# Kernel optimization log

Measured on AMD Instinct MI355X. Metric: run time of the kernel, lower is better.

## Reference

```python
import jax, jax.numpy as jnp
import numpy as np

N, M = 1024, 32
FN, FE = 64, 32
AGG_N, AGG_E = 128, 64
OUT_N, OUT_E = 64, 32


def _build_indices(n, m):
    nip, eip = [], []
    k = 0
    for i in range(1, n):
        j0 = max(0, i - m)
        nip += list(range(j0, i))
        eip += list(range(k, k + i - j0))
        k += i - j0
    n1 = np.array(nip, np.int32)
    eT = np.array(eip, np.int32)
    n2 = np.concatenate([np.full(min(i, m), i, np.int32) for i in range(1, n)])
    # padded previous-node window indices (0 = zero pad slot)
    prev_nodes = np.zeros(n * m, np.int32)
    k = 0
    for i in range(n):
        t = min(i, m)
        prev_nodes[(i + 1) * m - t:(i + 1) * m] = np.arange(k, k + t) + 1
        k += t
    n_e = k
    norm_node = np.full(n, 1.0 / m, np.float32)
    for i in range(1, m):
        norm_node[i] = 1.0 / i
    prev_edges = np.zeros(n_e * m, np.int32)
    k = 0
    e = 0
    for i in range(n):
        j0 = max(0, i - m)
        for j in range(j0, i):
            if j > j0:
                prev_edges[(e + 1) * m - (j - j0):(e + 1) * m] = np.arange(k, k + j - j0) + 1
            e += 1
        k += i - j0
    norm_edge = np.ones(n_e, np.float32)
    k = 0
    for i in range(1, n):
        t = min(i, m)
        for j in range(t):
            if j > 0:
                norm_edge[k] = 1.0 / j
            k += 1
    return n1, eT, n2, prev_nodes, norm_node, prev_edges, norm_edge, n_e

N1, ET, N2, PREV_N, NORM_N, PREV_E, NORM_E, NE = _build_indices(N, M)
N1 = jnp.asarray(N1); ET = jnp.asarray(ET); N2 = jnp.asarray(N2)
PREV_N = jnp.asarray(PREV_N); PREV_E = jnp.asarray(PREV_E)
NORM_N = jnp.asarray(NORM_N); NORM_E = jnp.asarray(NORM_E)


def setup_inputs() -> dict:
    key = jax.random.key(0)
    ks = jax.random.split(key, 20)
    s = 0.02
    inp = {
        'input_nodes': jax.random.normal(ks[0], (2, N, FN), jnp.float32),
        'input_edges': jax.random.normal(ks[1], (2, NE, FE), jnp.float32),
        # node-branch MLPs (exclude_last=False)
        'Wan1': jax.random.normal(ks[2], (2 * FN + FE, 2 * AGG_N)) * s,
        'ban1': jnp.zeros((2 * AGG_N,)),
        'Wan2': jax.random.normal(ks[3], (2 * AGG_N, AGG_N)) * s,
        'ban2': jnp.zeros((AGG_N,)),
        'Wln1': jax.random.normal(ks[4], (AGG_N + FN, AGG_N + FN)) * s,
        'bln1': jnp.zeros((AGG_N + FN,)),
        'Wln2': jax.random.normal(ks[5], (AGG_N + FN, OUT_N)) * s,
        'bln2': jnp.zeros((OUT_N,)),
        # edge-branch MLPs
        'Wae1': jax.random.normal(ks[6], (FN + FE, 2 * AGG_E)) * s,
        'bae1': jnp.zeros((2 * AGG_E,)),
        'Wae2': jax.random.normal(ks[7], (2 * AGG_E, AGG_E)) * s,
        'bae2': jnp.zeros((AGG_E,)),
        'Wle1': jax.random.normal(ks[8], (AGG_E + FE, AGG_E + FE)) * s,
        'ble1': jnp.zeros((AGG_E + FE,)),
        'Wle2': jax.random.normal(ks[9], (AGG_E + FE, OUT_E)) * s,
        'ble2': jnp.zeros((OUT_E,)),
    }
    return inp


def _mlp2(x, W1, b1, W2, b2):
    return jax.nn.relu(jax.nn.relu(x @ W1 + b1) @ W2 + b2)


def reference(input_nodes, input_edges, Wan1, ban1, Wan2, ban2, Wln1, bln1, Wln2, bln2,
              Wae1, bae1, Wae2, bae2, Wle1, ble1, Wle2, ble2):
    B = input_nodes.shape[0]
    # gather node-edge pairs [B, NE, FN+FE] and node-edge-node triples [B, NE, 2FN+FE]
    pairs = jnp.concatenate([input_nodes[:, N1], input_edges[:, ET]], axis=-1)
    triples = jnp.concatenate([input_nodes[:, N1], input_edges[:, ET], input_nodes[:, N2]], axis=-1)
    # node branch (exclude_last=False -> triples)
    hn = _mlp2(triples, Wan1, ban1, Wan2, ban2)                     # [B, NE, AGG_N]
    hn = jnp.concatenate([jnp.zeros((B, 1, AGG_N), hn.dtype), hn], axis=1)
    pn = hn[:, PREV_N].reshape(B, N, M, AGG_N).sum(axis=2)          # padded window sum
    pn = pn * NORM_N[None, :, None]
    nodes_in = jnp.concatenate([pn, input_nodes], axis=-1)
    out_nodes = _mlp2(nodes_in, Wln1, bln1, Wln2, bln2)             # activation_nodes = relu
    # edge branch (pairs)
    he = _mlp2(pairs, Wae1, bae1, Wae2, bae2)                       # [B, NE, AGG_E]
    he = jnp.concatenate([jnp.zeros((B, 1, AGG_E), he.dtype), he], axis=1)
    pe = he[:, PREV_E].reshape(B, NE, M, AGG_E).sum(axis=2)
    pe = pe * NORM_E[None, :, None]
    edges_in = jnp.concatenate([pe, input_edges], axis=-1)
    out_edges = _mlp2(edges_in, Wle1, ble1, Wle2, ble2)             # activation_edges = relu
    return out_nodes, out_edges
```

## Files before the change

kernel.cpp:

```cpp
#include <hip/hip_runtime.h>
#include <cstdint>

#define NN    1024
#define MM    32
#define NEDGE 32240
#define MROWS 64480
#define PX    168
#define PSTN  264
#define PXE   104
#define PH1   136
#define PHE   72

typedef unsigned short ushort_t;

typedef __bf16 bf16x8 __attribute__((ext_vector_type(8)));
typedef float  floatx4 __attribute__((ext_vector_type(4)));

__device__ __forceinline__ float b2f(ushort_t u) {
    union { unsigned int i; float f; } v; v.i = ((unsigned int)u) << 16; return v.f;
}
__device__ __forceinline__ ushort_t f2b(float f) {
    unsigned int u = __builtin_bit_cast(unsigned int, f);
    u = (u + 0x7FFFu + ((u >> 16) & 1u)) >> 16;
    return (ushort_t)u;
}
__device__ __forceinline__ int edge_base(int i) {
    return (i <= MM) ? ((i * (i - 1)) >> 1) : (496 + (i - MM) * MM);
}

__global__ __launch_bounds__(256) void k_pack(
        const float* an1, const float* an2, const float* ae1, const float* ae2,
        const float* le1, const float* le2, const float* ln1, const float* ln2,
        const float* nodes, const float* edges,
        ushort_t* pan1, ushort_t* pan2, ushort_t* pae1, ushort_t* pae2,
        ushort_t* ple1, ushort_t* ple2, ushort_t* pln1, ushort_t* pln2,
        ushort_t* nodesb, ushort_t* edgesb) {
    __shared__ float tile[32][33];
    const int bid = blockIdx.x;
    const int tid = threadIdx.x;
    if (bid < 152) {
        const float* s; ushort_t* d; int K, N, t;
        if (bid < 40)       { s = an1; d = pan1; K = 160; N = 256; t = bid;       }
        else if (bid < 72)  { s = an2; d = pan2; K = 256; N = 128; t = bid - 40;  }
        else if (bid < 84)  { s = ae1; d = pae1; K = 96;  N = 128; t = bid - 72;  }
        else if (bid < 92)  { s = ae2; d = pae2; K = 128; N = 64;  t = bid - 84;  }
        else if (bid < 101) { s = le1; d = ple1; K = 96;  N = 96;  t = bid - 92;  }
        else if (bid < 104) { s = le2; d = ple2; K = 96;  N = 32;  t = bid - 101; }
        else if (bid < 140) { s = ln1; d = pln1; K = 192; N = 192; t = bid - 104; }
        else                { s = ln2; d = pln2; K = 192; N = 64;  t = bid - 140; }
        int ntn = N >> 5;
        int tk = t / ntn, tn = t - tk * ntn;
        int k0 = tk * 32, n0 = tn * 32;
        int tx = tid & 31, ty = tid >> 5;
#pragma unroll
        for (int m = 0; m < 4; ++m)
            tile[ty + m * 8][tx] = s[(size_t)(k0 + ty + m * 8) * N + n0 + tx];
        __syncthreads();
#pragma unroll
        for (int m = 0; m < 4; ++m)
            d[(size_t)(n0 + ty + m * 8) * K + k0 + tx] = f2b(tile[tx][ty + m * 8]);
    } else if (bid < 280) {
        int i4 = (bid - 152) * 256 + tid;
        float4 v = ((const float4*)nodes)[i4];
        uint2 o;
        o.x = (unsigned)f2b(v.x) | ((unsigned)f2b(v.y) << 16);
        o.y = (unsigned)f2b(v.z) | ((unsigned)f2b(v.w) << 16);
        ((uint2*)nodesb)[i4] = o;
    } else {
        int i4 = (bid - 280) * 256 + tid;
        if (i4 < 515840) {
            float4 v = ((const float4*)edges)[i4];
            uint2 o;
            o.x = (unsigned)f2b(v.x) | ((unsigned)f2b(v.y) << 16);
            o.y = (unsigned)f2b(v.z) | ((unsigned)f2b(v.w) << 16);
            ((uint2*)edgesb)[i4] = o;
        }
    }
}

__global__ __launch_bounds__(512, 4) void k_main(
        const ushort_t* __restrict__ nodesb, const ushort_t* __restrict__ edgesb,
        const ushort_t* __restrict__ pan1, const float* __restrict__ ban1,
        const ushort_t* __restrict__ pan2, const float* __restrict__ ban2,
        const ushort_t* __restrict__ pae1, const float* __restrict__ bae1,
        const ushort_t* __restrict__ pae2, const float* __restrict__ bae2,
        const ushort_t* __restrict__ ple1, const float* __restrict__ ble1,
        const ushort_t* __restrict__ ple2, const float* __restrict__ ble2,
        ushort_t* __restrict__ pn, float* __restrict__ out_edges) {
    __shared__ alignas(16) ushort_t SH[26624];
    const int tid = threadIdx.x;
    const int w = tid >> 6, l = tid & 63, lrow = l & 15, lq = l >> 4;
    const int bid = blockIdx.x;
    floatx4 zero = {0.f, 0.f, 0.f, 0.f};

    if (bid < 2048) {
        const int b = bid >> 10, i = bid & 1023;
        const int t = min(i, MM);
        if (i == 0) {
            if (tid < 64) ((unsigned*)(pn + (size_t)bid * 128))[tid] = 0u;
            return;
        }
        const int j0 = i - t;
        const int base = b * NEDGE + edge_base(i);
        ushort_t* X = SH;
        ushort_t* H = SH + 32 * PX;

        bf16x8 B0[5], B1[5];
#pragma unroll
        for (int kt = 0; kt < 5; ++kt) {
            B0[kt] = *(const bf16x8*)(pan1 + (size_t)(16 * w + lrow) * 160 + kt * 32 + lq * 8);
            B1[kt] = *(const bf16x8*)(pan1 + (size_t)(16 * (w + 8) + lrow) * 160 + kt * 32 + lq * 8);
        }
        float c0 = ban1[16 * w + lrow];
        float c1 = ban1[16 * (w + 8) + lrow];

#pragma unroll
        for (int k = 0; k < 4; ++k) {
            int rr = w * 4 + k;
            unsigned* xr = (unsigned*)(X + rr * PX);
            const unsigned* nj = (const unsigned*)(nodesb + (size_t)(b * NN + j0 + rr) * 64);
            const unsigned* ni = (const unsigned*)(nodesb + (size_t)(b * NN + i) * 64);
            const unsigned* eb = (const unsigned*)(edgesb + (size_t)(base + rr) * 32);
            if (l < 32) { xr[l] = nj[l]; xr[48 + l] = ni[l]; }
            else        xr[l] = eb[l - 32];
        }
        __syncthreads();

#pragma unroll
        for (int s = 0; s < 2; ++s) {
            bf16x8 A[5];
#pragma unroll
            for (int kt = 0; kt < 5; ++kt)
                A[kt] = *(const bf16x8*)&X[(s * 16 + lrow) * PX + kt * 32 + lq * 8];
            floatx4 a0 = zero, a1 = zero;
#pragma unroll
            for (int kt = 0; kt < 5; ++kt) {
                a0 = __builtin_amdgcn_mfma_f32_16x16x32_bf16(A[kt], B0[kt], a0, 0, 0, 0);
                a1 = __builtin_amdgcn_mfma_f32_16x16x32_bf16(A[kt], B1[kt], a1, 0, 0, 0);
            }
#pragma unroll
            for (int r_ = 0; r_ < 4; ++r_) {
                int row = (s * 16 + lq * 4 + r_) * PSTN;
                H[row + 16 * w + lrow]       = f2b(fmaxf(a0[r_] + c0, 0.f));
                H[row + 128 + 16 * w + lrow] = f2b(fmaxf(a1[r_] + c1, 0.f));
            }
        }
        __syncthreads();

        {
            bf16x8 D[8];
#pragma unroll
            for (int kt = 0; kt < 8; ++kt)
                D[kt] = *(const bf16x8*)(pan2 + (size_t)(16 * w + lrow) * 256 + kt * 32 + lq * 8);
            float d0 = ban2[16 * w + lrow];
#pragma unroll
            for (int s = 0; s < 2; ++s) {
                floatx4 a0 = zero;
#pragma unroll
                for (int kt = 0; kt < 8; ++kt) {
                    bf16x8 a = *(const bf16x8*)&H[(s * 16 + lrow) * PSTN + kt * 32 + lq * 8];
                    a0 = __builtin_amdgcn_mfma_f32_16x16x32_bf16(a, D[kt], a0, 0, 0, 0);
                }
#pragma unroll
                for (int r_ = 0; r_ < 4; ++r_)
                    X[(s * 16 + lq * 4 + r_) * 136 + 16 * w + lrow] = f2b(fmaxf(a0[r_] + d0, 0.f));
            }
        }
        __syncthreads();

        {
            int c = tid & 63, g = tid >> 6;
            float s0 = 0.f, s1 = 0.f;
            for (int p = g; p < t; p += 8) {
                unsigned u = ((const unsigned*)X)[p * 68 + c];
                s0 += b2f((ushort_t)(u & 0xffff));
                s1 += b2f((ushort_t)(u >> 16));
            }
            float* red = (float*)(SH + 32 * PX);
            red[g * 128 + 2 * c]     = s0;
            red[g * 128 + 2 * c + 1] = s1;
            __syncthreads();
            if (tid < 64) {
                float inv = 1.0f / (float)t;
                float a0 = 0.f, a1 = 0.f;
#pragma unroll
                for (int g2 = 0; g2 < 8; ++g2) {
                    a0 += red[g2 * 128 + 2 * tid];
                    a1 += red[g2 * 128 + 2 * tid + 1];
                }
                a0 *= inv; a1 *= inv;
                ((unsigned*)(pn + (size_t)bid * 128))[tid] =
                    (unsigned)f2b(a0) | ((unsigned)f2b(a1) << 16);
            }
        }
    } else {
        const int q = bid - 2048;
        const int h = w >> 2, w4 = w & 3;
        const int lt = tid & 255;
        const int ri = 2 * q + h;
        const int b = ri >> 10, i = ri & 1023;
        const int t = min(i, MM);
        const int j0 = i - t;
        const int base = b * NEDGE + edge_base(i);
        ushort_t* Xe = SH + h * 13312;
        ushort_t* H1 = Xe + 3328;
        ushort_t* HE = H1 + 4352;
        ushort_t* LB = HE + 2304;

        bf16x8 B0[3], B1[3];
#pragma unroll
        for (int kt = 0; kt < 3; ++kt) {
            B0[kt] = *(const bf16x8*)(pae1 + (size_t)(16 * w4 + lrow) * 96 + kt * 32 + lq * 8);
            B1[kt] = *(const bf16x8*)(pae1 + (size_t)(16 * (w4 + 4) + lrow) * 96 + kt * 32 + lq * 8);
        }
        const float c0 = bae1[16 * w4 + lrow];
        const float c1 = bae1[16 * (w4 + 4) + lrow];

        for (int u = lt; u < 32 * 48; u += 256) {
            int row = u / 48, c = u - row * 48;
            unsigned v;
            if (c < 32) v = ((const unsigned*)nodesb)[(size_t)(b * NN + j0 + row) * 32 + c];
            else        v = ((const unsigned*)edgesb)[(size_t)(base + row) * 16 + (c - 32)];
            ((unsigned*)Xe)[row * (PXE / 2) + c] = v;
        }
        __syncthreads();

#pragma unroll
        for (int s = 0; s < 2; ++s) {
            bf16x8 A[3];
#pragma unroll
            for (int kt = 0; kt < 3; ++kt)
                A[kt] = *(const bf16x8*)&Xe[(s * 16 + lrow) * PXE + kt * 32 + lq * 8];
            floatx4 a0 = zero, a1 = zero;
#pragma unroll
            for (int kt = 0; kt < 3; ++kt) {
                a0 = __builtin_amdgcn_mfma_f32_16x16x32_bf16(A[kt], B0[kt], a0, 0, 0, 0);
                a1 = __builtin_amdgcn_mfma_f32_16x16x32_bf16(A[kt], B1[kt], a1, 0, 0, 0);
            }
#pragma unroll
            for (int r_ = 0; r_ < 4; ++r_) {
                int row = (s * 16 + lq * 4 + r_) * PH1;
                H1[row + 16 * w4 + lrow]      = f2b(fmaxf(a0[r_] + c0, 0.f));
                H1[row + 64 + 16 * w4 + lrow] = f2b(fmaxf(a1[r_] + c1, 0.f));
            }
        }
        __syncthreads();

        {
            bf16x8 E[4];
#pragma unroll
            for (int kt = 0; kt < 4; ++kt)
                E[kt] = *(const bf16x8*)(pae2 + (size_t)(16 * w4 + lrow) * 128 + kt * 32 + lq * 8);
            float d2 = bae2[16 * w4 + lrow];
#pragma unroll
            for (int s = 0; s < 2; ++s) {
                floatx4 a2 = zero;
#pragma unroll
                for (int kt = 0; kt < 4; ++kt) {
                    bf16x8 a = *(const bf16x8*)&H1[(s * 16 + lrow) * PH1 + kt * 32 + lq * 8];
                    a2 = __builtin_amdgcn_mfma_f32_16x16x32_bf16(a, E[kt], a2, 0, 0, 0);
                }
#pragma unroll
                for (int r_ = 0; r_ < 4; ++r_)
                    HE[(s * 16 + lq * 4 + r_) * PHE + 16 * w4 + lrow] = f2b(fmaxf(a2[r_] + d2, 0.f));
            }
        }
        if (l < 16) {
            float run = 0.f;
            for (int p = 0; p < t; ++p) {
                Xe[p * PXE + 16 * w4 + l] = f2b((p == 0) ? 0.f : run / (float)p);
                run += b2f(HE[p * PHE + 16 * w4 + l]);
            }
        }
        __syncthreads();

        {
            bf16x8 F0[3], F1[3];
            const bool two = (w4 < 2);
#pragma unroll
            for (int kt = 0; kt < 3; ++kt) {
                F0[kt] = *(const bf16x8*)(ple1 + (size_t)(16 * w4 + lrow) * 96 + kt * 32 + lq * 8);
                if (two)
                    F1[kt] = *(const bf16x8*)(ple1 + (size_t)(16 * (w4 + 4) + lrow) * 96 + kt * 32 + lq * 8);
            }
            float v0 = ble1[16 * w4 + lrow];
            float v1 = two ? ble1[16 * (w4 + 4) + lrow] : 0.f;
#pragma unroll
            for (int s = 0; s < 2; ++s) {
                bf16x8 A[3];
#pragma unroll
                for (int kt = 0; kt < 3; ++kt)
                    A[kt] = *(const bf16x8*)&Xe[(s * 16 + lrow) * PXE + kt * 32 + lq * 8];
                floatx4 a0 = zero, a1 = zero;
#pragma unroll
                for (int kt = 0; kt < 3; ++kt) {
                    a0 = __builtin_amdgcn_mfma_f32_16x16x32_bf16(A[kt], F0[kt], a0, 0, 0, 0);
                    if (two)
                        a1 = __builtin_amdgcn_mfma_f32_16x16x32_bf16(A[kt], F1[kt], a1, 0, 0, 0);
                }
#pragma unroll
                for (int r_ = 0; r_ < 4; ++r_) {
                    int row = (s * 16 + lq * 4 + r_) * PXE;
                    LB[row + 16 * w4 + lrow] = f2b(fmaxf(a0[r_] + v0, 0.f));
                    if (two)
                        LB[row + 64 + 16 * w4 + lrow] = f2b(fmaxf(a1[r_] + v1, 0.f));
                }
            }
        }
        __syncthreads();

        {
            int ct = w4 & 1, s = w4 >> 1;
            int c0o = 16 * ct;
            bf16x8 F2[3];
#pragma unroll
            for (int kt = 0; kt < 3; ++kt)
                F2[kt] = *(const bf16x8*)(ple2 + (size_t)(c0o + lrow) * 96 + kt * 32 + lq * 8);
            float v2 = ble2[c0o + lrow];
            floatx4 a2 = zero;
#pragma unroll
            for (int kt = 0; kt < 3; ++kt) {
                bf16x8 a = *(const bf16x8*)&LB[(s * 16 + lrow) * PXE + kt * 32 + lq * 8];
                a2 = __builtin_amdgcn_mfma_f32_16x16x32_bf16(a, F2[kt], a2, 0, 0, 0);
            }
#pragma unroll
            for (int r_ = 0; r_ < 4; ++r_) {
                int grow = s * 16 + lq * 4 + r_;
                if (grow < t)
                    out_edges[(size_t)(base + grow) * 32 + c0o + lrow] = fmaxf(a2[r_] + v2, 0.f);
            }
        }
    }
}

__global__ __launch_bounds__(192) void k_final(
        const ushort_t* __restrict__ pn, const ushort_t* __restrict__ nodesb,
        const ushort_t* __restrict__ pln1, const float* __restrict__ bln1,
        const ushort_t* __restrict__ pln2, const float* __restrict__ bln2,
        float* __restrict__ out_nodes) {
    __shared__ alignas(16) ushort_t LA[32 * 200];
    __shared__ alignas(16) ushort_t LB[32 * 200];
    const int tid = threadIdx.x;
    const int w = tid >> 6, l = tid & 63, lrow = l & 15, lq = l >> 4;
    floatx4 zero = {0.f, 0.f, 0.f, 0.f};

    int tile = blockIdx.x;
    for (int u = tid; u < 768; u += 192) {
        int row = u / 24, c = u - row * 24;
        int r = tile * 32 + row;
        const uint4* src = (c < 16) ? ((const uint4*)(pn + (size_t)r * 128) + c)
                                    : ((const uint4*)(nodesb + (size_t)r * 64) + (c - 16));
        *(uint4*)&LA[row * 200 + c * 8] = *src;
    }
    bf16x8 f1[6][4]; float v1[4];
#pragma unroll
    for (int kt = 0; kt < 6; ++kt)
#pragma unroll
        for (int nt = 0; nt < 4; ++nt)
            f1[kt][nt] = *(const bf16x8*)(pln1 + (size_t)(w * 64 + nt * 16 + lrow) * 192 + kt * 32 + lq * 8);
#pragma unroll
    for (int nt = 0; nt < 4; ++nt) v1[nt] = bln1[w * 64 + nt * 16 + lrow];
    __syncthreads();

    floatx4 acc[2][4];
#pragma unroll
    for (int s = 0; s < 2; ++s)
#pragma unroll
        for (int nt = 0; nt < 4; ++nt) acc[s][nt] = zero;
#pragma unroll
    for (int s = 0; s < 2; ++s)
#pragma unroll
        for (int kt = 0; kt < 6; ++kt) {
            bf16x8 a = *(const bf16x8*)&LA[(s * 16 + lrow) * 200 + kt * 32 + lq * 8];
#pragma unroll
            for (int nt = 0; nt < 4; ++nt)
                acc[s][nt] = __builtin_amdgcn_mfma_f32_16x16x32_bf16(a, f1[kt][nt], acc[s][nt], 0, 0, 0);
        }
#pragma unroll
    for (int s = 0; s < 2; ++s)
#pragma unroll
        for (int nt = 0; nt < 4; ++nt) {
            int col = w * 64 + nt * 16 + lrow;
#pragma unroll
            for (int r_ = 0; r_ < 4; ++r_)
                LB[(s * 16 + lq * 4 + r_) * 200 + col] = f2b(fmaxf(acc[s][nt][r_] + v1[nt], 0.f));
        }
    bf16x8 f2[6][2]; float v2[2] = {0.f, 0.f};
    if (w < 2) {
#pragma unroll
        for (int kt = 0; kt < 6; ++kt)
#pragma unroll
            for (int nt = 0; nt < 2; ++nt)
                f2[kt][nt] = *(const bf16x8*)(pln2 + (size_t)(w * 32 + nt * 16 + lrow) * 192 + kt * 32 + lq * 8);
#pragma unroll
        for (int nt = 0; nt < 2; ++nt) v2[nt] = bln2[w * 32 + nt * 16 + lrow];
    }
    __syncthreads();
    if (w < 2) {
        floatx4 a2[2][2];
#pragma unroll
        for (int s = 0; s < 2; ++s) { a2[s][0] = zero; a2[s][1] = zero; }
#pragma unroll
        for (int s = 0; s < 2; ++s)
#pragma unroll
            for (int kt = 0; kt < 6; ++kt) {
                bf16x8 a = *(const bf16x8*)&LB[(s * 16 + lrow) * 200 + kt * 32 + lq * 8];
#pragma unroll
                for (int nt = 0; nt < 2; ++nt)
                    a2[s][nt] = __builtin_amdgcn_mfma_f32_16x16x32_bf16(a, f2[kt][nt], a2[s][nt], 0, 0, 0);
            }
#pragma unroll
        for (int s = 0; s < 2; ++s)
#pragma unroll
            for (int nt = 0; nt < 2; ++nt) {
                int col = w * 32 + nt * 16 + lrow;
#pragma unroll
                for (int r_ = 0; r_ < 4; ++r_)
                    out_nodes[(size_t)(tile * 32 + s * 16 + lq * 4 + r_) * 64 + col] =
                        fmaxf(a2[s][nt][r_] + v2[nt], 0.f);
            }
    }
}

extern "C" void kernel_launch(void* const* d_in, const int* in_sizes, int n_in,
                              void* d_out, int out_size, void* d_ws, size_t ws_size,
                              hipStream_t stream) {
    const float* nodes = (const float*)d_in[0];
    const float* edges = (const float*)d_in[1];
    const float* Wan1 = (const float*)d_in[2];  const float* ban1 = (const float*)d_in[3];
    const float* Wan2 = (const float*)d_in[4];  const float* ban2 = (const float*)d_in[5];
    const float* Wln1 = (const float*)d_in[6];  const float* bln1 = (const float*)d_in[7];
    const float* Wln2 = (const float*)d_in[8];  const float* bln2 = (const float*)d_in[9];
    const float* Wae1 = (const float*)d_in[10]; const float* bae1 = (const float*)d_in[11];
    const float* Wae2 = (const float*)d_in[12]; const float* bae2 = (const float*)d_in[13];
    const float* Wle1 = (const float*)d_in[14]; const float* ble1 = (const float*)d_in[15];
    const float* Wle2 = (const float*)d_in[16]; const float* ble2 = (const float*)d_in[17];

    char* ws = (char*)d_ws;
    size_t o = 0;
    auto alloc = [&](size_t bytes) -> void* {
        void* r = ws + o;
        o += (bytes + 255) & ~(size_t)255;
        return r;
    };
    ushort_t* pn     = (ushort_t*)alloc((size_t)2048 * 128 * 2);
    ushort_t* nodesb = (ushort_t*)alloc((size_t)2 * NN * 64 * 2);
    ushort_t* edgesb = (ushort_t*)alloc((size_t)MROWS * 32 * 2);
    ushort_t* pan1 = (ushort_t*)alloc(160 * 256 * 2);
    ushort_t* pan2 = (ushort_t*)alloc(256 * 128 * 2);
    ushort_t* pae1 = (ushort_t*)alloc(96 * 128 * 2);
    ushort_t* pae2 = (ushort_t*)alloc(128 * 64 * 2);
    ushort_t* ple1 = (ushort_t*)alloc(96 * 96 * 2);
    ushort_t* ple2 = (ushort_t*)alloc(96 * 32 * 2);
    ushort_t* pln1 = (ushort_t*)alloc(192 * 192 * 2);
    ushort_t* pln2 = (ushort_t*)alloc(192 * 64 * 2);

    float* out_nodes = (float*)d_out;
    float* out_edges = (float*)d_out + 2 * NN * 64;

    k_pack<<<2296, 256, 0, stream>>>(Wan1, Wan2, Wae1, Wae2, Wle1, Wle2, Wln1, Wln2,
                                     nodes, edges,
                                     pan1, pan2, pae1, pae2, ple1, ple2, pln1, pln2,
                                     nodesb, edgesb);
    k_main<<<3072, 512, 0, stream>>>(nodesb, edgesb,
                                     pan1, ban1, pan2, ban2,
                                     pae1, bae1, pae2, bae2,
                                     ple1, ble1, ple2, ble2,
                                     pn, out_edges);
    k_final<<<64, 192, 0, stream>>>(pn, nodesb, pln1, bln1, pln2, bln2, out_nodes);

    (void)in_sizes; (void)n_in; (void)out_size; (void)ws_size;
}
```

Measured before the change: 158.5 us.

## Reduce window sum in registers and shrink LDS to raise occupancy

The node branch now sums the second-layer MLP outputs over the window directly in registers with wave shuffles. This replaces the LDS write, the extra barrier and the two-stage shared-memory reduction. The edge branch reuses the H1 region for LB, so the shared array shrinks and launch bounds ask for 8 blocks per CU instead of 4. The bf16 conversion now uses the native cast, which may differ in NaN handling, and the tighter launch bound may force register spills.

```diff
diff --git a/kernel.cpp b/kernel.cpp
--- a/kernel.cpp
+++ b/kernel.cpp
@@ -10,6 +10,7 @@
 #define PXE   104
 #define PH1   136
 #define PHE   72
+#define EHALF 9984
 
 typedef unsigned short ushort_t;
 
@@ -20,9 +21,7 @@
     union { unsigned int i; float f; } v; v.i = ((unsigned int)u) << 16; return v.f;
 }
 __device__ __forceinline__ ushort_t f2b(float f) {
-    unsigned int u = __builtin_bit_cast(unsigned int, f);
-    u = (u + 0x7FFFu + ((u >> 16) & 1u)) >> 16;
-    return (ushort_t)u;
+    return __builtin_bit_cast(ushort_t, (__bf16)f);
 }
 __device__ __forceinline__ int edge_base(int i) {
     return (i <= MM) ? ((i * (i - 1)) >> 1) : (496 + (i - MM) * MM);
@@ -78,7 +77,7 @@
     }
 }
 
-__global__ __launch_bounds__(512, 4) void k_main(
+__global__ __launch_bounds__(512, 8) void k_main(
         const ushort_t* __restrict__ nodesb, const ushort_t* __restrict__ edgesb,
         const ushort_t* __restrict__ pan1, const float* __restrict__ ban1,
         const ushort_t* __restrict__ pan2, const float* __restrict__ ban2,
@@ -87,7 +86,7 @@
         const ushort_t* __restrict__ ple1, const float* __restrict__ ble1,
         const ushort_t* __restrict__ ple2, const float* __restrict__ ble2,
         ushort_t* __restrict__ pn, float* __restrict__ out_edges) {
-    __shared__ alignas(16) ushort_t SH[26624];
+    __shared__ alignas(16) ushort_t SH[2 * EHALF];
     const int tid = threadIdx.x;
     const int w = tid >> 6, l = tid & 63, lrow = l & 15, lq = l >> 4;
     const int bid = blockIdx.x;
@@ -153,6 +152,7 @@
             for (int kt = 0; kt < 8; ++kt)
                 D[kt] = *(const bf16x8*)(pan2 + (size_t)(16 * w + lrow) * 256 + kt * 32 + lq * 8);
             float d0 = ban2[16 * w + lrow];
+            float P = 0.f;
 #pragma unroll
             for (int s = 0; s < 2; ++s) {
                 floatx4 a0 = zero;
@@ -162,36 +162,17 @@
                     a0 = __builtin_amdgcn_mfma_f32_16x16x32_bf16(a, D[kt], a0, 0, 0, 0);
                 }
 #pragma unroll
-                for (int r_ = 0; r_ < 4; ++r_)
-                    X[(s * 16 + lq * 4 + r_) * 136 + 16 * w + lrow] = f2b(fmaxf(a0[r_] + d0, 0.f));
-            }
-        }
-        __syncthreads();
-
-        {
-            int c = tid & 63, g = tid >> 6;
-            float s0 = 0.f, s1 = 0.f;
-            for (int p = g; p < t; p += 8) {
-                unsigned u = ((const unsigned*)X)[p * 68 + c];
-                s0 += b2f((ushort_t)(u & 0xffff));
-                s1 += b2f((ushort_t)(u >> 16));
-            }
-            float* red = (float*)(SH + 32 * PX);
-            red[g * 128 + 2 * c]     = s0;
-            red[g * 128 + 2 * c + 1] = s1;
-            __syncthreads();
-            if (tid < 64) {
-                float inv = 1.0f / (float)t;
-                float a0 = 0.f, a1 = 0.f;
-#pragma unroll
-                for (int g2 = 0; g2 < 8; ++g2) {
-                    a0 += red[g2 * 128 + 2 * tid];
-                    a1 += red[g2 * 128 + 2 * tid + 1];
+                for (int r_ = 0; r_ < 4; ++r_) {
+                    int row = s * 16 + lq * 4 + r_;
+                    float v = fmaxf(a0[r_] + d0, 0.f);
+                    float vr = b2f(f2b(v));
+                    if (row < t) P += vr;
                 }
-                a0 *= inv; a1 *= inv;
-                ((unsigned*)(pn + (size_t)bid * 128))[tid] =
-                    (unsigned)f2b(a0) | ((unsigned)f2b(a1) << 16);
-            }
+            }
+            P += __shfl_xor(P, 16);
+            P += __shfl_xor(P, 32);
+            if (l < 16)
+                pn[(size_t)bid * 128 + 16 * w + lrow] = f2b(P * (1.0f / (float)t));
         }
     } else {
         const int q = bid - 2048;
@@ -202,10 +183,10 @@
         const int t = min(i, MM);
         const int j0 = i - t;
         const int base = b * NEDGE + edge_base(i);
-        ushort_t* Xe = SH + h * 13312;
+        ushort_t* Xe = SH + h * EHALF;
         ushort_t* H1 = Xe + 3328;
         ushort_t* HE = H1 + 4352;
-        ushort_t* LB = HE + 2304;
+        ushort_t* LB = H1;
 
         bf16x8 B0[3], B1[3];
 #pragma unroll
```

Result: slower. 168.9 us (+6.5%).
